# Performance work log

Measured on AMD Instinct MI355X. Metric: run time of the kernel, lower is better.

The kernel has to match this reference:

```python
import jax, jax.numpy as jnp
import numpy as np

L = 5          # number of pyramid levels (cat_fuse expects 5*C input channels)
C = 192        # in_channels, divisible by 3 and 2
C3 = C // 3
C2 = C // 2
B = 4
SIZES = [(192, 192), (96, 96), (48, 48), (24, 24), (12, 12)]  # x[1] is reference scale


def conv1x1(x, w, b):
    # 1x1 conv (+ folded eval-mode BN): x [n,cin,h,w], w [cout,cin], b [cout]
    return jnp.einsum('oc,nchw->nohw', w, x) + b[None, :, None, None]


def setup_inputs() -> dict:
    key = jax.random.key(0)
    ks = iter(jax.random.split(key, 40))
    inp = {}
    for i, (h, w) in enumerate(SIZES):
        inp[f'x{i}'] = jax.random.normal(next(ks), (B, C, h, w), jnp.float32)
    def wp(shape):
        return jax.random.normal(next(ks), shape, jnp.float32) * 0.05
    for nm, co, ci in [('k1', C3, C), ('k2', C3, C), ('k3', C3, C), ('q', C, C), ('v', C, C),
                       ('cf', C, L * C), ('e1', C2, C), ('e2', C, C2), ('r1', C2, C), ('r2', C, C2)]:
        inp['W_' + nm] = wp((co, ci))
        inp['b_' + nm] = wp((co,))
    inp['bn_s'] = 1.0 + wp((C,))   # standalone BN folded to affine scale
    inp['bn_t'] = wp((C,))         # standalone BN folded to affine shift
    return inp


def reference(x0, x1, x2, x3, x4,
              W_k1, b_k1, W_k2, b_k2, W_k3, b_k3,
              W_q, b_q, W_v, b_v, W_cf, b_cf,
              W_e1, b_e1, W_e2, b_e2, W_r1, b_r1, W_r2, b_r2,
              bn_s, bn_t):
    xs = [x0, x1, x2, x3, x4]
    b, _, h, w = x1.shape
    hw = h * w
    # bilinear resize to reference scale (torch F.interpolate align_corners=False)
    x_up = [x1 if i == 1 else jax.image.resize(x, (b, C, h, w), 'bilinear') for i, x in enumerate(xs)]
    Xf = jnp.stack(x_up).reshape(L * b, C, h, w)  # shared weights across levels -> batch them

    def emb(z):  # conv1x1 -> GELU(exact) -> conv1x1 (dropout is identity at eval)
        return conv1x1(jax.nn.gelu(conv1x1(z, W_e1, b_e1), approximate=False), W_e2, b_e2)

    la_res = None
    for k in range(5):
        # residual refinement: relu(bn(x + res_block(x)))
        r = conv1x1(jax.nn.relu(conv1x1(Xf, W_r1, b_r1)), W_r2, b_r2)
        Xf = jax.nn.relu((Xf + r) * bn_s[None, :, None, None] + bn_t[None, :, None, None])
        # query/value: per-level projection, split C into 3 chunks -> 15 'keys' per pixel
        Q = conv1x1(Xf, W_q, b_q).reshape(L, b, 3, C3, hw)
        Q = Q.transpose(1, 0, 2, 3, 4).reshape(b, 3 * L, C3, hw).transpose(0, 3, 2, 1)  # [b,hw,C3,15]
        V = conv1x1(Xf, W_v, b_v).reshape(L, b, 3, C3, hw)
        V = V.transpose(1, 0, 2, 3, 4).reshape(b, 3 * L, C3, hw).transpose(0, 3, 1, 2)  # [b,hw,15,C3]
        if k == 0:
            cat = Xf.reshape(L, b, C, h, w).transpose(1, 0, 2, 3, 4).reshape(b, L * C, h, w)
            la_res = emb(jax.nn.relu(conv1x1(cat, W_cf, b_cf)))
        refs = []
        for Wk, bk in ((W_k1, b_k1), (W_k2, b_k2), (W_k3, b_k3)):
            key_i = conv1x1(la_res, Wk, bk).reshape(b, C3, hw).transpose(0, 2, 1)       # [b,hw,C3]
            att = jax.nn.softmax(jnp.einsum('bpc,bpck->bpk', key_i, Q), axis=-1)        # [b,hw,15]
            ref = jnp.einsum('bpk,bpkc->bpc', att, V)                                   # [b,hw,C3]
            refs.append(ref.transpose(0, 2, 1).reshape(b, C3, h, w))
        la_res = emb(jnp.concatenate(refs, axis=1))
    return la_res
```

## Files before the change

kernel.cpp:

```cpp
#include <hip/hip_runtime.h>
#include <math.h>

typedef unsigned short u16;
typedef unsigned int   u32;
typedef __bf16 bf16x8 __attribute__((ext_vector_type(8)));
typedef float  f32x4  __attribute__((ext_vector_type(4)));

__device__ __forceinline__ float b2f(u16 u) {
    unsigned v = ((unsigned)u) << 16;
    return __uint_as_float(v);
}
__device__ __forceinline__ u16 f2b(float f) {
    unsigned x = __float_as_uint(f);
    unsigned r = (x + 0x7fffu + ((x >> 16) & 1u)) >> 16;
    return (u16)r;
}
__device__ __forceinline__ void fsplit(float v, u16& h, u16& l) {
    h = f2b(v);
    l = f2b(v - b2f(h));
}
__device__ __forceinline__ float h2f(u16 u) {
    union { u16 us; _Float16 h; } c; c.us = u; return (float)c.h;
}
__device__ __forceinline__ u16 f2h(float f) {
    union { u16 us; _Float16 h; } c; c.h = (_Float16)f; return c.us;
}
__device__ __forceinline__ float ldx(const void* p, size_t i, int f32m) {
    return f32m ? ((const float*)p)[i] : b2f(((const u16*)p)[i]);
}

__device__ __forceinline__ void gld16(u16* l, const u16* g) {
    __builtin_amdgcn_global_load_lds(
        (const __attribute__((address_space(1))) unsigned int*)g,
        (__attribute__((address_space(3))) unsigned int*)l,
        16, 0, 0);
}

__device__ __forceinline__ int swz(int row) {
    return (row & 3) ^ ((row >> 2) & 3);
}

__global__ void detect_dtype(const u16* __restrict__ x0, int* flag)
{
    int lane = threadIdx.x;
    int bad = 0;
    for (int i = lane; i < 1024; i += 64) {
        float v = b2f(x0[i]);
        if (!(fabsf(v) < 32768.f)) bad = 1;
    }
    unsigned long long m = __ballot(bad);
    if (lane == 0) flag[0] = (m != 0ULL) ? 1 : 0;
}

struct SrcPtrs {
    const void *wr1, *br1, *wr2, *br2, *wq, *bq, *wv, *bv, *wcf, *bcf;
    const void *we1, *be1, *we2, *be2, *wk1, *bk1, *wk2, *bk2, *wk3, *bk3;
    const void *bns, *bnt;
};
__global__ void pack_weights(SrcPtrs S, u16* __restrict__ Wh, u16* __restrict__ Wl,
                             float* __restrict__ Bias, const int* __restrict__ dflag)
{
    const int f32m = *dflag;
    int idx = blockIdx.x * 256 + threadIdx.x;
    if (idx < 368640) {
        const void* src; size_t si;
        if (idx < 18432)       { src = S.wr1; si = idx; }
        else if (idx < 36864)  { src = S.wr2; si = idx - 18432; }
        else if (idx < 110592) {
            int r = idx - 36864, o = r / 192, c = r % 192;
            if (o < 192) { src = S.wq; si = (size_t)o * 192 + c; }
            else         { src = S.wv; si = (size_t)(o - 192) * 192 + c; }
        }
        else if (idx < 294912) { src = S.wcf; si = idx - 110592; }
        else if (idx < 313344) { src = S.we1; si = idx - 294912; }
        else if (idx < 331776) { src = S.we2; si = idx - 313344; }
        else {
            int r = idx - 331776, o = r / 192, c = r % 192;
            src = (o < 64) ? S.wk1 : ((o < 128) ? S.wk2 : S.wk3);
            si = (size_t)(o & 63) * 192 + c;
        }
        u16 h, l; fsplit(ldx(src, si, f32m), h, l);
        Wh[idx] = h; Wl[idx] = l;
    } else if (idx < 370368) {
        int b = idx - 368640; const void* src; size_t si;
        if (b < 96)        { src = S.br1; si = b; }
        else if (b < 288)  { src = S.br2; si = b - 96; }
        else if (b < 672)  { int r = b - 288;
                             if (r < 192) { src = S.bq; si = r; }
                             else         { src = S.bv; si = r - 192; } }
        else if (b < 864)  { src = S.bcf; si = b - 672; }
        else if (b < 960)  { src = S.be1; si = b - 864; }
        else if (b < 1152) { src = S.be2; si = b - 960; }
        else if (b < 1344) { int r = b - 1152;
                             src = (r < 64) ? S.bk1 : ((r < 128) ? S.bk2 : S.bk3);
                             si = r & 63; }
        else if (b < 1536) { src = S.bns; si = b - 1344; }
        else               { src = S.bnt; si = b - 1536; }
        Bias[b] = ldx(src, si, f32m);
    }
}

__global__ void build_tables(float* __restrict__ wtab, int* __restrict__ jtab)
{
    int t = threadIdx.x;
    if (t >= 384) return;
    int li = t / 96, o = t % 96;
    const int ins[4] = {192, 48, 24, 12};
    int in = ins[li];
    float scale = (float)in / 96.0f;
    float ksc = fmaxf(scale, 1.0f);
    float cc = (o + 0.5f) * scale - 0.5f;
    float w[4] = {0.f, 0.f, 0.f, 0.f};
    int   j[4] = {0, 0, 0, 0};
    int n = 0; float s = 0.f;
    int jl = (int)floorf(cc - ksc), jh = (int)floorf(cc + ksc) + 1;
    for (int jj = jl; jj <= jh; jj++) {
        if (jj < 0 || jj >= in) continue;
        float ww = 1.0f - fabsf((float)jj - cc) / ksc;
        if (ww <= 0.f) continue;
        if (n < 4) { w[n] = ww; j[n] = jj; s += ww; n++; }
    }
    for (int i = 0; i < 4; i++) {
        wtab[li * 384 + o * 4 + i] = w[i] / s;
        jtab[li * 384 + o * 4 + i] = j[i];
    }
}

template<int SPLIT>
__launch_bounds__(256)
__global__ void transpose_in(const void* __restrict__ src, int HW,
                             u32* __restrict__ P, u16* __restrict__ Xh,
                             u16* __restrict__ Xl, const int* __restrict__ dflag)
{
    __shared__ float t[32][33];
    const int f32m = *dflag;
    const int b  = blockIdx.z;
    const int c0 = blockIdx.y * 32;
    const int p0 = blockIdx.x * 32;
    const int tid = threadIdx.x;
#pragma unroll
    for (int it = 0; it < 4; it++) {
        int i = it * 256 + tid;
        int pl = i & 31, cl = i >> 5;
        int p = p0 + pl;
        float v = 0.f;
        if (p < HW) v = ldx(src, ((size_t)(b * 192 + c0 + cl)) * HW + p, f32m);
        t[pl][cl] = v;
    }
    __syncthreads();
#pragma unroll
    for (int it = 0; it < 4; it++) {
        int i = it * 256 + tid;
        int cl = i & 31, pl = i >> 5;
        int p = p0 + pl;
        if (p >= HW) continue;
        float v = t[pl][cl];
        u16 h, l; fsplit(v, h, l);
        if constexpr (SPLIT) {
            size_t oi = ((size_t)((4 + b) * 9216 + p)) * 192 + c0 + cl;
            Xh[oi] = h; Xl[oi] = l;
        } else {
            P[((size_t)b * HW + p) * 192 + c0 + cl] = (u32)h | ((u32)l << 16);
        }
    }
}

template<int TAPS>
__launch_bounds__(256)
__global__ void upsample2(const u32* __restrict__ Pa, const u32* __restrict__ Pb,
                          const u32* __restrict__ Pc,
                          const float* __restrict__ wtab, const int* __restrict__ jtab,
                          u16* __restrict__ Xh, u16* __restrict__ Xl)
{
    int li, b, l, in;
    const u32* P;
    if constexpr (TAPS == 4) {
        li = 0; b = blockIdx.y; l = 0; in = 192; P = Pa;
    } else {
        int yi = blockIdx.y;
        li = 1 + (yi >> 2); b = yi & 3;
        const int lvl[4] = {0, 2, 3, 4};
        const int ins[4] = {192, 48, 24, 12};
        l = lvl[li]; in = ins[li];
        P = (li == 1) ? Pa : ((li == 2) ? Pb : Pc);
    }
    int gid = blockIdx.x * 256 + threadIdx.x;
    int c = gid % 192;
    int p = gid / 192;
    int y = p / 96, x = p % 96;
    const float* wt = wtab + li * 384;
    const int*   jt = jtab + li * 384;

    size_t ib = (size_t)b * in * in * 192 + c;
    float a = 0.f;
#pragma unroll
    for (int iy = 0; iy < TAPS; iy++) {
        float wy = wt[y * 4 + iy];
        size_t rb = ib + (size_t)(jt[y * 4 + iy] * in) * 192;
        float ax = 0.f;
#pragma unroll
        for (int ix = 0; ix < TAPS; ix++) {
            u32 u = P[rb + jt[x * 4 + ix] * 192];
            ax += wt[x * 4 + ix] * (b2f((u16)u) + b2f((u16)(u >> 16)));
        }
        a += wy * ax;
    }
    size_t oi = ((size_t)(l * 4 + b) * 9216 + p) * 192 + c;
    u16 h, lo; fsplit(a, h, lo);
    Xh[oi] = h; Xl[oi] = lo;
}

template<int MT, int NT, int ACT, int MODE, int OUT>
__launch_bounds__(256)
__global__ void conv_gemm(const u16* __restrict__ Ah, const u16* __restrict__ Al,
                          const u16* __restrict__ Wh, const u16* __restrict__ Wl,
                          const float* __restrict__ Bias,
                          int woff, int boff, int K, int O,
                          u16* __restrict__ out0, u16* __restrict__ out1)
{
    constexpr int BM = MT * 64, BN = NT * 16;
    __shared__ u16 Ash[BM * 40];
    __shared__ u16 Asl[BM * 40];
    __shared__ u16 Bsh[BN * 40];
    __shared__ u16 Bsl[BN * 40];

    const int tid  = threadIdx.x;
    const int lane = tid & 63, wave = tid >> 6;
    const int qd   = lane >> 4, ln = lane & 15;
    const int p0   = blockIdx.x * BM;
    const int img  = blockIdx.z;
    const int M    = 9216;

    f32x4 acc[MT][NT];
#pragma unroll
    for (int mt = 0; mt < MT; mt++)
#pragma unroll
        for (int j = 0; j < NT; j++) acc[mt][j] = (f32x4){0.f, 0.f, 0.f, 0.f};

    for (int kb = 0; kb < K; kb += 32) {
#pragma unroll
        for (int i = 0; i < MT; i++) {
            int idx = i * 256 + tid;
            int row = idx >> 2, ch = idx & 3;
            size_t base;
            if constexpr (MODE == 2) {
                int l = kb / 192, c0 = kb - l * 192 + ch * 8;
                base = ((size_t)((l * 4 + img) * M + p0 + row)) * 192 + c0;
            } else {
                base = ((size_t)(img * M + p0 + row)) * (size_t)K + kb + ch * 8;
            }
            *(float4*)&Ash[row * 40 + ch * 8] = *(const float4*)(Ah + base);
            *(float4*)&Asl[row * 40 + ch * 8] = *(const float4*)(Al + base);
        }
        constexpr int BI = (BN * 4) / 256;
#pragma unroll
        for (int i = 0; i < BI; i++) {
            int idx = i * 256 + tid;
            int row = idx >> 2, ch = idx & 3;
            size_t wb = (size_t)woff + (size_t)row * K + kb + ch * 8;
            *(float4*)&Bsh[row * 40 + ch * 8] = *(const float4*)(Wh + wb);
            *(float4*)&Bsl[row * 40 + ch * 8] = *(const float4*)(Wl + wb);
        }
        __syncthreads();
        bf16x8 ah[MT], al[MT];
#pragma unroll
        for (int mt = 0; mt < MT; mt++) {
            ah[mt] = *(const bf16x8*)&Ash[(wave * MT * 16 + mt * 16 + ln) * 40 + qd * 8];
            al[mt] = *(const bf16x8*)&Asl[(wave * MT * 16 + mt * 16 + ln) * 40 + qd * 8];
        }
#pragma unroll
        for (int j = 0; j < NT; j++) {
            bf16x8 bh = *(const bf16x8*)&Bsh[(j * 16 + ln) * 40 + qd * 8];
            bf16x8 bl = *(const bf16x8*)&Bsl[(j * 16 + ln) * 40 + qd * 8];
#pragma unroll
            for (int mt = 0; mt < MT; mt++) {
                acc[mt][j] = __builtin_amdgcn_mfma_f32_16x16x32_bf16(ah[mt], bh, acc[mt][j], 0, 0, 0);
                acc[mt][j] = __builtin_amdgcn_mfma_f32_16x16x32_bf16(ah[mt], bl, acc[mt][j], 0, 0, 0);
                acc[mt][j] = __builtin_amdgcn_mfma_f32_16x16x32_bf16(al[mt], bh, acc[mt][j], 0, 0, 0);
            }
        }
        __syncthreads();
    }

#pragma unroll
    for (int mt = 0; mt < MT; mt++) {
#pragma unroll
        for (int j = 0; j < NT; j++) {
            int o = j * 16 + ln;
            float bvf = Bias[boff + o];
#pragma unroll
            for (int r = 0; r < 4; r++) {
                int prow = p0 + wave * MT * 16 + mt * 16 + qd * 4 + r;
                float v = acc[mt][j][r] + bvf;
                if constexpr (ACT == 1) v = fmaxf(v, 0.f);
                if constexpr (OUT == 0) {
                    size_t oidx = ((size_t)(img * M + prow)) * (size_t)O + o;
                    u16 h, l; fsplit(v, h, l);
                    out0[oidx] = h; out1[oidx] = l;
                } else if constexpr (OUT == 1) {
                    out0[((size_t)(img * M + prow)) * (size_t)O + o] = f2h(v);
                } else {
                    size_t pb = ((size_t)(img * M + prow)) * 192;
                    if (o < 192) out0[pb + o] = f2h(v);
                    else         out1[pb + o - 192] = f2h(v);
                }
            }
        }
    }
}

template<int ACT1, int MODE2>
__launch_bounds__(256)
__global__ void fused_mlp(const u16* __restrict__ Ah, const u16* __restrict__ Al,
                          const u16* __restrict__ Wh, const u16* __restrict__ Wl,
                          const float* __restrict__ Bias,
                          int w1off, int b1off, int w2off, int b2off,
                          u16* __restrict__ outh, u16* __restrict__ outl)
{
    __shared__ __align__(16) u16 LDS[38912];
    u16* Hh = LDS;
    u16* Hl = LDS + 6656;

    const int tid  = threadIdx.x;
    const int lane = tid & 63, wave = tid >> 6;
    const int qd   = lane >> 4, ln = lane & 15;
    const int p0   = blockIdx.x * 64;
    const int img  = blockIdx.z;
    const int M    = 9216;
    const int irow = tid >> 2, ich = tid & 3;

    auto g1issue = [&](int kb, int c) {
        u16* SA = LDS + 13312 + c * 10240;
        int ch = ich ^ swz(irow);
        size_t ga = ((size_t)(img * M + p0 + irow)) * 192 + kb + ch * 8;
        gld16(SA + wave * 512,        Ah + ga);
        gld16(SA + 2048 + wave * 512, Al + ga);
        size_t gb = (size_t)w1off + (size_t)irow * 192 + kb + ch * 8;
        gld16(SA + 4096 + wave * 512, Wh + gb);
        gld16(SA + 7168 + wave * 512, Wl + gb);
        if (tid < 128) {
            int r2 = 64 + irow;
            int ch2 = ich ^ swz(r2);
            size_t gb2 = (size_t)w1off + (size_t)r2 * 192 + kb + ch2 * 8;
            gld16(SA + 6144 + wave * 512, Wh + gb2);
            gld16(SA + 9216 + wave * 512, Wl + gb2);
        }
    };
    auto g2issue = [&](int kb, int c) {
        u16* B2 = LDS + 13312 + c * 12288;
#pragma unroll
        for (int i = 0; i < 3; i++) {
            int r = i * 64 + irow;
            int ch = ich ^ swz(r);
            size_t g = (size_t)w2off + (size_t)r * 96 + kb + ch * 8;
            gld16(B2 + i * 2048 + wave * 512,        Wh + g);
            gld16(B2 + 6144 + i * 2048 + wave * 512, Wl + g);
        }
    };

    f32x4 acc1[6];
#pragma unroll
    for (int j = 0; j < 6; j++) acc1[j] = (f32x4){0.f, 0.f, 0.f, 0.f};

    g1issue(0, 0);
    __syncthreads();
#pragma unroll 2
    for (int kb = 0; kb < 192; kb += 32) {
        int cur = (kb >> 5) & 1;
        if (kb + 32 < 192) g1issue(kb + 32, cur ^ 1);
        const u16* SA = LDS + 13312 + cur * 10240;
        int arow = wave * 16 + ln;
        int asl = arow * 32 + ((qd ^ swz(arow)) << 3);
        bf16x8 ah = *(const bf16x8*)&SA[asl];
        bf16x8 al = *(const bf16x8*)&SA[2048 + asl];
#pragma unroll
        for (int j = 0; j < 6; j++) {
            int brow = j * 16 + ln;
            int bsl = brow * 32 + ((qd ^ swz(brow)) << 3);
            bf16x8 bh = *(const bf16x8*)&SA[4096 + bsl];
            bf16x8 bl = *(const bf16x8*)&SA[7168 + bsl];
            acc1[j] = __builtin_amdgcn_mfma_f32_16x16x32_bf16(ah, bh, acc1[j], 0, 0, 0);
            acc1[j] = __builtin_amdgcn_mfma_f32_16x16x32_bf16(ah, bl, acc1[j], 0, 0, 0);
            acc1[j] = __builtin_amdgcn_mfma_f32_16x16x32_bf16(al, bh, acc1[j], 0, 0, 0);
        }
        __syncthreads();
    }

    g2issue(0, 0);
#pragma unroll
    for (int j = 0; j < 6; j++) {
        int o = j * 16 + ln;
        float bvf = Bias[b1off + o];
#pragma unroll
        for (int r = 0; r < 4; r++) {
            float v = acc1[j][r] + bvf;
            if constexpr (ACT1 == 1) v = fmaxf(v, 0.f);
            if constexpr (ACT1 == 2) v = 0.5f * v * (1.f + erff(v * 0.70710678118654752f));
            u16 h, l; fsplit(v, h, l);
            int row = wave * 16 + qd * 4 + r;
            Hh[row * 104 + o] = h;
            Hl[row * 104 + o] = l;
        }
    }
    __syncthreads();

    f32x4 acc2[12];
#pragma unroll
    for (int j = 0; j < 12; j++) acc2[j] = (f32x4){0.f, 0.f, 0.f, 0.f};

#pragma unroll
    for (int kb = 0; kb < 96; kb += 32) {
        int cur = (kb >> 5) & 1;
        if (kb + 32 < 96) g2issue(kb + 32, cur ^ 1);
        const u16* B2 = LDS + 13312 + cur * 12288;
        bf16x8 ah = *(const bf16x8*)&Hh[(wave * 16 + ln) * 104 + kb + qd * 8];
        bf16x8 al = *(const bf16x8*)&Hl[(wave * 16 + ln) * 104 + kb + qd * 8];
#pragma unroll
        for (int j = 0; j < 12; j++) {
            int brow = j * 16 + ln;
            int bsl = brow * 32 + ((qd ^ swz(brow)) << 3);
            bf16x8 bh = *(const bf16x8*)&B2[bsl];
            bf16x8 bl = *(const bf16x8*)&B2[6144 + bsl];
            acc2[j] = __builtin_amdgcn_mfma_f32_16x16x32_bf16(ah, bh, acc2[j], 0, 0, 0);
            acc2[j] = __builtin_amdgcn_mfma_f32_16x16x32_bf16(ah, bl, acc2[j], 0, 0, 0);
            acc2[j] = __builtin_amdgcn_mfma_f32_16x16x32_bf16(al, bh, acc2[j], 0, 0, 0);
        }
        __syncthreads();
    }

#pragma unroll
    for (int j = 0; j < 12; j++) {
        int o = j * 16 + ln;
        float bvf = Bias[b2off + o];
#pragma unroll
        for (int r = 0; r < 4; r++) {
            int prow = p0 + wave * 16 + qd * 4 + r;
            float v = acc2[j][r] + bvf;
            size_t oidx = ((size_t)(img * M + prow)) * 192 + o;
            if constexpr (MODE2 == 1) {
                float xo = b2f(outh[oidx]) + b2f(outl[oidx]);
                v = fmaxf((xo + v) * Bias[1344 + o] + Bias[1536 + o], 0.f);
            }
            u16 h, l; fsplit(v, h, l);
            outh[oidx] = h; outl[oidx] = l;
        }
    }
}

template<int WRITE_X>
__launch_bounds__(256)
__global__ void fused_res_qv(u16* __restrict__ Xh, u16* __restrict__ Xl,
                             const u16* __restrict__ Wh, const u16* __restrict__ Wl,
                             const float* __restrict__ Bias,
                             u16* __restrict__ Qf, u16* __restrict__ Vf)
{
    __shared__ __align__(16) u16 LDS[38912];
    u16* Hh = LDS;
    u16* Hl = LDS + 6656;

    const int tid  = threadIdx.x;
    const int lane = tid & 63, wave = tid >> 6;
    const int qd   = lane >> 4, ln = lane & 15;
    const int p0   = blockIdx.x * 64;
    const int img  = blockIdx.z;
    const int M    = 9216;
    const int irow = tid >> 2, ich = tid & 3;

    auto g1issue = [&](int kb, int c) {
        u16* SA = LDS + 13312 + c * 10240;
        int ch = ich ^ swz(irow);
        size_t ga = ((size_t)(img * M + p0 + irow)) * 192 + kb + ch * 8;
        gld16(SA + wave * 512,        Xh + ga);
        gld16(SA + 2048 + wave * 512, Xl + ga);
        size_t gb = (size_t)irow * 192 + kb + ch * 8;
        gld16(SA + 4096 + wave * 512, Wh + gb);
        gld16(SA + 7168 + wave * 512, Wl + gb);
        if (tid < 128) {
            int r2 = 64 + irow;
            int ch2 = ich ^ swz(r2);
            size_t gb2 = (size_t)r2 * 192 + kb + ch2 * 8;
            gld16(SA + 6144 + wave * 512, Wh + gb2);
            gld16(SA + 9216 + wave * 512, Wl + gb2);
        }
    };
    auto g2issue = [&](int kb, int c) {
        u16* B2 = LDS + 13312 + c * 12288;
#pragma unroll
        for (int i = 0; i < 3; i++) {
            int r = i * 64 + irow;
            int ch = ich ^ swz(r);
            size_t g = (size_t)18432 + (size_t)r * 96 + kb + ch * 8;
            gld16(B2 + i * 2048 + wave * 512,        Wh + g);
            gld16(B2 + 6144 + i * 2048 + wave * 512, Wl + g);
        }
    };
    auto g3issue = [&](int s, int c) {
        int p = s / 6, kb = (s - p * 6) * 32;
        u16* B3 = LDS + 24576 + c * 6144;
        int ch = ich ^ swz(irow);
        size_t g = (size_t)36864 + (size_t)(p * 96 + irow) * 192 + kb + ch * 8;
        gld16(B3 + wave * 512,        Wh + g);
        gld16(B3 + 3072 + wave * 512, Wl + g);
        if (tid < 128) {
            int r2 = 64 + irow;
            int ch2 = ich ^ swz(r2);
            size_t g2 = (size_t)36864 + (size_t)(p * 96 + r2) * 192 + kb + ch2 * 8;
            gld16(B3 + 2048 + wave * 512, Wh + g2);
            gld16(B3 + 5120 + wave * 512, Wl + g2);
        }
    };

    f32x4 acc1[6];
#pragma unroll
    for (int j = 0; j < 6; j++) acc1[j] = (f32x4){0.f, 0.f, 0.f, 0.f};

    g1issue(0, 0);
    __syncthreads();
#pragma unroll 2
    for (int kb = 0; kb < 192; kb += 32) {
        int cur = (kb >> 5) & 1;
        if (kb + 32 < 192) g1issue(kb + 32, cur ^ 1);
        const u16* SA = LDS + 13312 + cur * 10240;
        int arow = wave * 16 + ln;
        int asl = arow * 32 + ((qd ^ swz(arow)) << 3);
        bf16x8 ah = *(const bf16x8*)&SA[asl];
        bf16x8 al = *(const bf16x8*)&SA[2048 + asl];
#pragma unroll
        for (int j = 0; j < 6; j++) {
            int brow = j * 16 + ln;
            int bsl = brow * 32 + ((qd ^ swz(brow)) << 3);
            bf16x8 bh = *(const bf16x8*)&SA[4096 + bsl];
            bf16x8 bl = *(const bf16x8*)&SA[7168 + bsl];
            acc1[j] = __builtin_amdgcn_mfma_f32_16x16x32_bf16(ah, bh, acc1[j], 0, 0, 0);
            acc1[j] = __builtin_amdgcn_mfma_f32_16x16x32_bf16(ah, bl, acc1[j], 0, 0, 0);
            acc1[j] = __builtin_amdgcn_mfma_f32_16x16x32_bf16(al, bh, acc1[j], 0, 0, 0);
        }
        __syncthreads();
    }

    g2issue(0, 0);
#pragma unroll
    for (int j = 0; j < 6; j++) {
        int o = j * 16 + ln;
        float bvf = Bias[o];
#pragma unroll
        for (int r = 0; r < 4; r++) {
            float v = fmaxf(acc1[j][r] + bvf, 0.f);
            u16 h, l; fsplit(v, h, l);
            int row = wave * 16 + qd * 4 + r;
            Hh[row * 104 + o] = h;
            Hl[row * 104 + o] = l;
        }
    }
    __syncthreads();

    f32x4 acc2[12];
#pragma unroll
    for (int j = 0; j < 12; j++) acc2[j] = (f32x4){0.f, 0.f, 0.f, 0.f};

#pragma unroll
    for (int kb = 0; kb < 96; kb += 32) {
        int cur = (kb >> 5) & 1;
        if (kb + 32 < 96) g2issue(kb + 32, cur ^ 1);
        const u16* B2 = LDS + 13312 + cur * 12288;
        bf16x8 ah = *(const bf16x8*)&Hh[(wave * 16 + ln) * 104 + kb + qd * 8];
        bf16x8 al = *(const bf16x8*)&Hl[(wave * 16 + ln) * 104 + kb + qd * 8];
#pragma unroll
        for (int j = 0; j < 12; j++) {
            int brow = j * 16 + ln;
            int bsl = brow * 32 + ((qd ^ swz(brow)) << 3);
            bf16x8 bh = *(const bf16x8*)&B2[bsl];
            bf16x8 bl = *(const bf16x8*)&B2[6144 + bsl];
            acc2[j] = __builtin_amdgcn_mfma_f32_16x16x32_bf16(ah, bh, acc2[j], 0, 0, 0);
            acc2[j] = __builtin_amdgcn_mfma_f32_16x16x32_bf16(ah, bl, acc2[j], 0, 0, 0);
            acc2[j] = __builtin_amdgcn_mfma_f32_16x16x32_bf16(al, bh, acc2[j], 0, 0, 0);
        }
        __syncthreads();
    }

    g3issue(0, 0);

    u16* X2h = LDS;
    u16* X2l = LDS + 12288;
#pragma unroll
    for (int j = 0; j < 12; j++) {
        int o = j * 16 + ln;
        float bvf = Bias[96 + o];
#pragma unroll
        for (int r = 0; r < 4; r++) {
            int row  = wave * 16 + qd * 4 + r;
            int prow = p0 + row;
            float v = acc2[j][r] + bvf;
            size_t oidx = ((size_t)(img * M + prow)) * 192 + o;
            float xo = b2f(Xh[oidx]) + b2f(Xl[oidx]);
            v = fmaxf((xo + v) * Bias[1344 + o] + Bias[1536 + o], 0.f);
            u16 h, l; fsplit(v, h, l);
            if constexpr (WRITE_X) { Xh[oidx] = h; Xl[oidx] = l; }
            int off = ((row * 192 + o) * 2) ^ ((row & 7) << 4);
            *(u16*)((char*)X2h + off) = h;
            *(u16*)((char*)X2l + off) = l;
        }
    }
    __syncthreads();

    const int arow = wave * 16 + ln;
#pragma unroll 1
    for (int pass = 0; pass < 4; pass++) {
        f32x4 acc3[6];
#pragma unroll
        for (int j = 0; j < 6; j++) acc3[j] = (f32x4){0.f, 0.f, 0.f, 0.f};

#pragma unroll 2
        for (int t6 = 0; t6 < 6; t6++) {
            int s = pass * 6 + t6;
            int cur = t6 & 1;
            if (s < 23) g3issue(s + 1, cur ^ 1);
            int kb = t6 * 32;
            int aoff = ((arow * 192 + kb + qd * 8) * 2) ^ ((arow & 7) << 4);
            bf16x8 ah = *(const bf16x8*)((const char*)X2h + aoff);
            bf16x8 al = *(const bf16x8*)((const char*)X2l + aoff);
            const u16* B3 = LDS + 24576 + cur * 6144;
#pragma unroll
            for (int j = 0; j < 6; j++) {
                int brow = j * 16 + ln;
                int bsl = brow * 32 + ((qd ^ swz(brow)) << 3);
                bf16x8 bh = *(const bf16x8*)&B3[bsl];
                bf16x8 bl = *(const bf16x8*)&B3[3072 + bsl];
                acc3[j] = __builtin_amdgcn_mfma_f32_16x16x32_bf16(ah, bh, acc3[j], 0, 0, 0);
                acc3[j] = __builtin_amdgcn_mfma_f32_16x16x32_bf16(ah, bl, acc3[j], 0, 0, 0);
                acc3[j] = __builtin_amdgcn_mfma_f32_16x16x32_bf16(al, bh, acc3[j], 0, 0, 0);
            }
            __syncthreads();
        }
#pragma unroll
        for (int j = 0; j < 6; j++) {
            int o = pass * 96 + j * 16 + ln;
            float bvf = Bias[288 + o];
#pragma unroll
            for (int r = 0; r < 4; r++) {
                int prow = p0 + wave * 16 + qd * 4 + r;
                float v = acc3[j][r] + bvf;
                u16 q = f2h(v);
                size_t pb = ((size_t)(img * M + prow)) * 192;
                if (o < 192) Qf[pb + o] = q;
                else         Vf[pb + o - 192] = q;
            }
        }
    }
}

__global__ void attn_kernel(const u16* __restrict__ Qb, const u16* __restrict__ Vb,
                            const u16* __restrict__ Keys,
                            u16* __restrict__ Rh, u16* __restrict__ Rl)
{
    const int lane = threadIdx.x & 63;
    const int wv   = threadIdx.x >> 6;
    const int p = blockIdx.x * 4 + wv;
    const int b = blockIdx.y;

    float qv[15], vv[15];
#pragma unroll
    for (int l = 0; l < 5; l++) {
        size_t base = ((size_t)((l * 4 + b) * 9216 + p)) * 192;
#pragma unroll
        for (int j = 0; j < 3; j++) {
            qv[l * 3 + j] = h2f(Qb[base + j * 64 + lane]);
            vv[l * 3 + j] = h2f(Vb[base + j * 64 + lane]);
        }
    }
    size_t kb = ((size_t)(b * 9216 + p)) * 192;
#pragma unroll
    for (int i = 0; i < 3; i++) {
        float kf = h2f(Keys[kb + i * 64 + lane]);
        float lg[15];
#pragma unroll
        for (int t = 0; t < 15; t++) {
            float s = kf * qv[t];
#pragma unroll
            for (int m = 1; m < 64; m <<= 1) s += __shfl_xor(s, m, 64);
            lg[t] = s;
        }
        float mx = lg[0];
#pragma unroll
        for (int t = 1; t < 15; t++) mx = fmaxf(mx, lg[t]);
        float sum = 0.f;
#pragma unroll
        for (int t = 0; t < 15; t++) { lg[t] = __expf(lg[t] - mx); sum += lg[t]; }
        float inv = 1.f / sum;
        float ref = 0.f;
#pragma unroll
        for (int t = 0; t < 15; t++) ref += lg[t] * vv[t];
        u16 h, lo; fsplit(ref * inv, h, lo);
        Rh[kb + i * 64 + lane] = h;
        Rl[kb + i * 64 + lane] = lo;
    }
}

__launch_bounds__(256)
__global__ void transpose_out(const u16* __restrict__ Lah, const u16* __restrict__ Lal,
                              float* __restrict__ out)
{
    __shared__ float t[32][33];
    const int b  = blockIdx.z;
    const int c0 = blockIdx.y * 32;
    const int p0 = blockIdx.x * 32;
    const int tid = threadIdx.x;
#pragma unroll
    for (int it = 0; it < 4; it++) {
        int i = it * 256 + tid;
        int cl = i & 31, pl = i >> 5;
        size_t idx = ((size_t)(b * 9216 + p0 + pl)) * 192 + c0 + cl;
        t[pl][cl] = b2f(Lah[idx]) + b2f(Lal[idx]);
    }
    __syncthreads();
#pragma unroll
    for (int it = 0; it < 4; it++) {
        int i = it * 256 + tid;
        int pl = i & 31, cl = i >> 5;
        out[((size_t)(b * 192 + c0 + cl)) * 9216 + p0 + pl] = t[pl][cl];
    }
}

__global__ void ws_too_small_kernel(float* out)
{
    int gid = blockIdx.x * 256 + threadIdx.x;
    out[gid] = 12345.0f;
}

extern "C" void kernel_launch(void* const* d_in, const int* in_sizes, int n_in,
                              void* d_out, int out_size, void* d_ws, size_t ws_size,
                              hipStream_t stream)
{
    u16* ws = (u16*)d_ws;
    const size_t oXh   = 0;
    const size_t oXl   = 35389440;
    const size_t oQ    = 70778880;
    const size_t oV    = 106168320;
    const size_t oLah  = 141557760;
    const size_t oLal  = 148635648;
    const size_t oKeys = 155713536;
    const size_t oRh   = 162791424;
    const size_t oRl   = 169869312;
    const size_t oWh   = 176947200;
    const size_t oWl   = 177315840;
    const size_t oBias = 177684480;
    const size_t oWtab = 177687936;
    const size_t oJtab = 177691008;
    const size_t oFlag = 177694080;
    const size_t need_bytes = (size_t)177694096 * 2;

    if (ws_size < need_bytes) {
        ws_too_small_kernel<<<dim3(out_size / 256), dim3(256), 0, stream>>>((float*)d_out);
        return;
    }

    u16* Xh   = ws + oXh;
    u16* Xl   = ws + oXl;
    u16* Qf   = ws + oQ;
    u16* Vf   = ws + oV;
    u16* Lah  = ws + oLah;
    u16* Lal  = ws + oLal;
    u16* Keys = ws + oKeys;
    u16* Rh   = ws + oRh;
    u16* Rl   = ws + oRl;
    u16* Wh   = ws + oWh;
    u16* Wl   = ws + oWl;
    float* Bias = (float*)(ws + oBias);
    float* wtab = (float*)(ws + oWtab);
    int*   jtab = (int*)(ws + oJtab);
    int*   flag = (int*)(ws + oFlag);

    u32* P0 = (u32*)(ws + oQ);
    u32* P2 = (u32*)(ws + oLah);
    u32* P3 = (u32*)(ws + oLal);
    u32* P4 = (u32*)(ws + oKeys);

    SrcPtrs S;
    S.wk1 = d_in[5];  S.bk1 = d_in[6];
    S.wk2 = d_in[7];  S.bk2 = d_in[8];
    S.wk3 = d_in[9];  S.bk3 = d_in[10];
    S.wq  = d_in[11]; S.bq  = d_in[12];
    S.wv  = d_in[13]; S.bv  = d_in[14];
    S.wcf = d_in[15]; S.bcf = d_in[16];
    S.we1 = d_in[17]; S.be1 = d_in[18];
    S.we2 = d_in[19]; S.be2 = d_in[20];
    S.wr1 = d_in[21]; S.br1 = d_in[22];
    S.wr2 = d_in[23]; S.br2 = d_in[24];
    S.bns = d_in[25]; S.bnt = d_in[26];

    dim3 blk(256);
    detect_dtype<<<dim3(1), dim3(64), 0, stream>>>((const u16*)d_in[0], flag);
    pack_weights<<<dim3(1447), blk, 0, stream>>>(S, Wh, Wl, Bias, flag);
    build_tables<<<dim3(1), dim3(384), 0, stream>>>(wtab, jtab);

    transpose_in<0><<<dim3(1152, 6, 4), blk, 0, stream>>>(d_in[0], 36864, P0, nullptr, nullptr, flag);
    transpose_in<1><<<dim3( 288, 6, 4), blk, 0, stream>>>(d_in[1],  9216, nullptr, Xh, Xl, flag);
    transpose_in<0><<<dim3(  72, 6, 4), blk, 0, stream>>>(d_in[2],  2304, P2, nullptr, nullptr, flag);
    transpose_in<0><<<dim3(  18, 6, 4), blk, 0, stream>>>(d_in[3],   576, P3, nullptr, nullptr, flag);
    transpose_in<0><<<dim3(   5, 6, 4), blk, 0, stream>>>(d_in[4],   144, P4, nullptr, nullptr, flag);
    upsample2<4><<<dim3(6912,  4), blk, 0, stream>>>(P0, nullptr, nullptr, wtab, jtab, Xh, Xl);
    upsample2<2><<<dim3(6912, 12), blk, 0, stream>>>(P2, P3, P4, wtab, jtab, Xh, Xl);

    for (int k = 0; k < 5; k++) {
        if (k < 4)
            fused_res_qv<1><<<dim3(144, 1, 20), blk, 0, stream>>>(
                Xh, Xl, Wh, Wl, Bias, Qf, Vf);
        else
            fused_res_qv<0><<<dim3(144, 1, 20), blk, 0, stream>>>(
                Xh, Xl, Wh, Wl, Bias, Qf, Vf);
        if (k == 0) {
            conv_gemm<2, 12, 1, 2, 0><<<dim3(72, 1, 4), blk, 0, stream>>>(
                Xh, Xl, Wh, Wl, Bias, 110592, 672, 960, 192, Rh, Rl);
            fused_mlp<2, 0><<<dim3(144, 1, 4), blk, 0, stream>>>(
                Rh, Rl, Wh, Wl, Bias, 294912, 864, 313344, 960, Lah, Lal);
        }
        conv_gemm<2, 12, 0, 0, 1><<<dim3(72, 1, 4), blk, 0, stream>>>(
            Lah, Lal, Wh, Wl, Bias, 331776, 1152, 192, 192, Keys, nullptr);
        attn_kernel<<<dim3(2304, 4), blk, 0, stream>>>(Qf, Vf, Keys, Rh, Rl);
        fused_mlp<2, 0><<<dim3(144, 1, 4), blk, 0, stream>>>(
            Rh, Rl, Wh, Wl, Bias, 294912, 864, 313344, 960, Lah, Lal);
    }
    transpose_out<<<dim3(288, 6, 4), blk, 0, stream>>>(Lah, Lal, (float*)d_out);
}
```

Before: 2.520 ms.

## Fuse key projection GEMM into the embedding MLP epilogue

The embedding MLP kernel now stages its 64x192 output tile (hi/lo bf16 split) in LDS. It then runs the key projection (three C3 heads, 192 outputs) directly from that tile, writing Keys in fp16. This removes the separate conv_gemm launch and its re-read of la_res from global memory each iteration. In exchange, the MLP kernel gets longer per block, adds an extra double-buffered weight stream and more LDS use, and skips the keys work on the last iteration.

Result: slower. 2.605 ms (+3.4%).

```diff
diff --git a/kernel.cpp b/kernel.cpp
--- a/kernel.cpp
+++ b/kernel.cpp
@@ -309,13 +309,14 @@
     }
 }
 
-template<int ACT1, int MODE2>
+template<int ACT1, int MODE2, int KEYS>
 __launch_bounds__(256)
 __global__ void fused_mlp(const u16* __restrict__ Ah, const u16* __restrict__ Al,
                           const u16* __restrict__ Wh, const u16* __restrict__ Wl,
                           const float* __restrict__ Bias,
                           int w1off, int b1off, int w2off, int b2off,
-                          u16* __restrict__ outh, u16* __restrict__ outl)
+                          u16* __restrict__ outh, u16* __restrict__ outl,
+                          u16* __restrict__ Keys)
 {
     __shared__ __align__(16) u16 LDS[38912];
     u16* Hh = LDS;
@@ -357,6 +358,21 @@
             gld16(B2 + 6144 + i * 2048 + wave * 512, Wl + g);
         }
     };
+    auto g3issue = [&](int s, int c) {
+        int p = s / 6, kb = (s - p * 6) * 32;
+        u16* B3 = LDS + 24576 + c * 6144;
+        int ch = ich ^ swz(irow);
+        size_t g = (size_t)331776 + (size_t)(p * 96 + irow) * 192 + kb + ch * 8;
+        gld16(B3 + wave * 512,        Wh + g);
+        gld16(B3 + 3072 + wave * 512, Wl + g);
+        if (tid < 128) {
+            int r2 = 64 + irow;
+            int ch2 = ich ^ swz(r2);
+            size_t g2 = (size_t)331776 + (size_t)(p * 96 + r2) * 192 + kb + ch2 * 8;
+            gld16(B3 + 2048 + wave * 512, Wh + g2);
+            gld16(B3 + 5120 + wave * 512, Wl + g2);
+        }
+    };
 
     f32x4 acc1[6];
 #pragma unroll
@@ -428,13 +444,18 @@
         __syncthreads();
     }
 
+    if constexpr (KEYS) g3issue(0, 0);
+
+    u16* X2h = LDS;
+    u16* X2l = LDS + 12288;
 #pragma unroll
     for (int j = 0; j < 12; j++) {
         int o = j * 16 + ln;
         float bvf = Bias[b2off + o];
 #pragma unroll
         for (int r = 0; r < 4; r++) {
-            int prow = p0 + wave * 16 + qd * 4 + r;
+            int row  = wave * 16 + qd * 4 + r;
+            int prow = p0 + row;
             float v = acc2[j][r] + bvf;
             size_t oidx = ((size_t)(img * M + prow)) * 192 + o;
             if constexpr (MODE2 == 1) {
@@ -443,6 +464,54 @@
             }
             u16 h, l; fsplit(v, h, l);
             outh[oidx] = h; outl[oidx] = l;
+            if constexpr (KEYS) {
+                int off = ((row * 192 + o) * 2) ^ ((row & 7) << 4);
+                *(u16*)((char*)X2h + off) = h;
+                *(u16*)((char*)X2l + off) = l;
+            }
+        }
+    }
+    if constexpr (!KEYS) return;
+    __syncthreads();
+
+    const int arow = wave * 16 + ln;
+#pragma unroll 1
+    for (int pass = 0; pass < 2; pass++) {
+        f32x4 acc3[6];
+#pragma unroll
+        for (int j = 0; j < 6; j++) acc3[j] = (f32x4){0.f, 0.f, 0.f, 0.f};
+
+#pragma unroll 2
+        for (int t6 = 0; t6 < 6; t6++) {
+            int s = pass * 6 + t6;
+            int cur = t6 & 1;
+            if (s < 11) g3issue(s + 1, cur ^ 1);
+            int kb = t6 * 32;
+            int aoff = ((arow * 192 + kb + qd * 8) * 2) ^ ((arow & 7) << 4);
+            bf16x8 ah = *(const bf16x8*)((const char*)X2h + aoff);
+            bf16x8 al = *(const bf16x8*)((const char*)X2l + aoff);
+            const u16* B3 = LDS + 24576 + cur * 6144;
+#pragma unroll
+            for (int j = 0; j < 6; j++) {
+                int brow = j * 16 + ln;
+                int bsl = brow * 32 + ((qd ^ swz(brow)) << 3);
+                bf16x8 bh = *(const bf16x8*)&B3[bsl];
+                bf16x8 bl = *(const bf16x8*)&B3[3072 + bsl];
+                acc3[j] = __builtin_amdgcn_mfma_f32_16x16x32_bf16(ah, bh, acc3[j], 0, 0, 0);
+                acc3[j] = __builtin_amdgcn_mfma_f32_16x16x32_bf16(ah, bl, acc3[j], 0, 0, 0);
+                acc3[j] = __builtin_amdgcn_mfma_f32_16x16x32_bf16(al, bh, acc3[j], 0, 0, 0);
+            }
+            __syncthreads();
+        }
+#pragma unroll
+        for (int j = 0; j < 6; j++) {
+            int o = pass * 96 + j * 16 + ln;
+            float bvf = Bias[1152 + o];
+#pragma unroll
+            for (int r = 0; r < 4; r++) {
+                int prow = p0 + wave * 16 + qd * 4 + r;
+                Keys[((size_t)(img * M + prow)) * 192 + o] = f2h(acc3[j][r] + bvf);
+            }
         }
     }
 }
@@ -811,14 +880,16 @@
         if (k == 0) {
             conv_gemm<2, 12, 1, 2, 0><<<dim3(72, 1, 4), blk, 0, stream>>>(
                 Xh, Xl, Wh, Wl, Bias, 110592, 672, 960, 192, Rh, Rl);
-            fused_mlp<2, 0><<<dim3(144, 1, 4), blk, 0, stream>>>(
-                Rh, Rl, Wh, Wl, Bias, 294912, 864, 313344, 960, Lah, Lal);
-        }
-        conv_gemm<2, 12, 0, 0, 1><<<dim3(72, 1, 4), blk, 0, stream>>>(
-            Lah, Lal, Wh, Wl, Bias, 331776, 1152, 192, 192, Keys, nullptr);
+            fused_mlp<2, 0, 1><<<dim3(144, 1, 4), blk, 0, stream>>>(
+                Rh, Rl, Wh, Wl, Bias, 294912, 864, 313344, 960, Lah, Lal, Keys);
+        }
         attn_kernel<<<dim3(2304, 4), blk, 0, stream>>>(Qf, Vf, Keys, Rh, Rl);
-        fused_mlp<2, 0><<<dim3(144, 1, 4), blk, 0, stream>>>(
-            Rh, Rl, Wh, Wl, Bias, 294912, 864, 313344, 960, Lah, Lal);
+        if (k < 4)
+            fused_mlp<2, 0, 1><<<dim3(144, 1, 4), blk, 0, stream>>>(
+                Rh, Rl, Wh, Wl, Bias, 294912, 864, 313344, 960, Lah, Lal, Keys);
+        else
+            fused_mlp<2, 0, 0><<<dim3(144, 1, 4), blk, 0, stream>>>(
+                Rh, Rl, Wh, Wl, Bias, 294912, 864, 313344, 960, Lah, Lal, nullptr);
     }
     transpose_out<<<dim3(288, 6, 4), blk, 0, stream>>>(Lah, Lal, (float*)d_out);
 }
```

## Double-buffer conv_gemm with async global-to-LDS loads and swizzled layout

Applied to the files above, without the earlier changes.

Rewrites conv_gemm to fetch the next K-slice straight into LDS (gld16) while the current slice feeds MFMA, using two LDS buffers and an XOR swizzle in place of padded rows. The M tile drops from 128 to 64 rows, doubling the grid to 144 blocks per image so more blocks are resident. The goal is to hide global load latency and cut LDS bank conflicts, at the cost of less A-fragment reuse per B load and 64KB of LDS per block.

Result: faster. 2.456 ms (-2.5%).

```diff
diff --git a/kernel.cpp b/kernel.cpp
--- a/kernel.cpp
+++ b/kernel.cpp
@@ -210,7 +210,7 @@
     Xh[oi] = h; Xl[oi] = lo;
 }
 
-template<int MT, int NT, int ACT, int MODE, int OUT>
+template<int NT, int ACT, int MODE, int OUT>
 __launch_bounds__(256)
 __global__ void conv_gemm(const u16* __restrict__ Ah, const u16* __restrict__ Al,
                           const u16* __restrict__ Wh, const u16* __restrict__ Wl,
@@ -218,92 +218,87 @@
                           int woff, int boff, int K, int O,
                           u16* __restrict__ out0, u16* __restrict__ out1)
 {
-    constexpr int BM = MT * 64, BN = NT * 16;
-    __shared__ u16 Ash[BM * 40];
-    __shared__ u16 Asl[BM * 40];
-    __shared__ u16 Bsh[BN * 40];
-    __shared__ u16 Bsl[BN * 40];
+    __shared__ __align__(16) u16 LDS[32768];
 
     const int tid  = threadIdx.x;
     const int lane = tid & 63, wave = tid >> 6;
     const int qd   = lane >> 4, ln = lane & 15;
-    const int p0   = blockIdx.x * BM;
+    const int p0   = blockIdx.x * 64;
     const int img  = blockIdx.z;
     const int M    = 9216;
-
-    f32x4 acc[MT][NT];
-#pragma unroll
-    for (int mt = 0; mt < MT; mt++)
-#pragma unroll
-        for (int j = 0; j < NT; j++) acc[mt][j] = (f32x4){0.f, 0.f, 0.f, 0.f};
-
+    const int irow = tid >> 2, ich = tid & 3;
+
+    auto issue = [&](int kb, int c) {
+        u16* S = LDS + c * 16384;
+        {
+            int ch = ich ^ swz(irow);
+            size_t ga;
+            if constexpr (MODE == 2) {
+                int l = kb / 192;
+                ga = ((size_t)((l * 4 + img) * M + p0 + irow)) * 192 + (kb - l * 192) + ch * 8;
+            } else {
+                ga = ((size_t)(img * M + p0 + irow)) * (size_t)K + kb + ch * 8;
+            }
+            gld16(S + wave * 512,        Ah + ga);
+            gld16(S + 2048 + wave * 512, Al + ga);
+        }
+#pragma unroll
+        for (int i = 0; i < 3; i++) {
+            int idx = i * 256 + tid;
+            int brow = idx >> 2;
+            int bc = (idx & 3) ^ swz(brow);
+            size_t gb = (size_t)woff + (size_t)brow * K + kb + bc * 8;
+            gld16(S + 4096 + i * 2048 + wave * 512,  Wh + gb);
+            gld16(S + 10240 + i * 2048 + wave * 512, Wl + gb);
+        }
+    };
+
+    f32x4 acc[NT];
+#pragma unroll
+    for (int j = 0; j < NT; j++) acc[j] = (f32x4){0.f, 0.f, 0.f, 0.f};
+
+    issue(0, 0);
+    __syncthreads();
     for (int kb = 0; kb < K; kb += 32) {
-#pragma unroll
-        for (int i = 0; i < MT; i++) {
-            int idx = i * 256 + tid;
-            int row = idx >> 2, ch = idx & 3;
-            size_t base;
-            if constexpr (MODE == 2) {
-                int l = kb / 192, c0 = kb - l * 192 + ch * 8;
-                base = ((size_t)((l * 4 + img) * M + p0 + row)) * 192 + c0;
+        int cur = (kb >> 5) & 1;
+        if (kb + 32 < K) issue(kb + 32, cur ^ 1);
+        const u16* S = LDS + cur * 16384;
+        int arow = wave * 16 + ln;
+        int asl = arow * 32 + ((qd ^ swz(arow)) << 3);
+        bf16x8 ah = *(const bf16x8*)&S[asl];
+        bf16x8 al = *(const bf16x8*)&S[2048 + asl];
+#pragma unroll
+        for (int j = 0; j < NT; j++) {
+            int brow = j * 16 + ln;
+            int bsl = brow * 32 + ((qd ^ swz(brow)) << 3);
+            bf16x8 bh = *(const bf16x8*)&S[4096 + bsl];
+            bf16x8 bl = *(const bf16x8*)&S[10240 + bsl];
+            acc[j] = __builtin_amdgcn_mfma_f32_16x16x32_bf16(ah, bh, acc[j], 0, 0, 0);
+            acc[j] = __builtin_amdgcn_mfma_f32_16x16x32_bf16(ah, bl, acc[j], 0, 0, 0);
+            acc[j] = __builtin_amdgcn_mfma_f32_16x16x32_bf16(al, bh, acc[j], 0, 0, 0);
+        }
+        __syncthreads();
+    }
+
+#pragma unroll
+    for (int j = 0; j < NT; j++) {
+        int o = j * 16 + ln;
+        float bvf = Bias[boff + o];
+#pragma unroll
+        for (int r = 0; r < 4; r++) {
+            int prow = p0 + wave * 16 + qd * 4 + r;
+            float v = acc[j][r] + bvf;
+            if constexpr (ACT == 1) v = fmaxf(v, 0.f);
+            if constexpr (OUT == 0) {
+                size_t oidx = ((size_t)(img * M + prow)) * (size_t)O + o;
+                u16 h, l; fsplit(v, h, l);
+                out0[oidx] = h; out1[oidx] = l;
+            } else if constexpr (OUT == 1) {
+                out0[((size_t)(img * M + prow)) * (size_t)O + o] = f2h(v);
             } else {
-                base = ((size_t)(img * M + p0 + row)) * (size_t)K + kb + ch * 8;
-            }
-            *(float4*)&Ash[row * 40 + ch * 8] = *(const float4*)(Ah + base);
-            *(float4*)&Asl[row * 40 + ch * 8] = *(const float4*)(Al + base);
-        }
-        constexpr int BI = (BN * 4) / 256;
-#pragma unroll
-        for (int i = 0; i < BI; i++) {
-            int idx = i * 256 + tid;
-            int row = idx >> 2, ch = idx & 3;
-            size_t wb = (size_t)woff + (size_t)row * K + kb + ch * 8;
-            *(float4*)&Bsh[row * 40 + ch * 8] = *(const float4*)(Wh + wb);
-            *(float4*)&Bsl[row * 40 + ch * 8] = *(const float4*)(Wl + wb);
-        }
-        __syncthreads();
-        bf16x8 ah[MT], al[MT];
-#pragma unroll
-        for (int mt = 0; mt < MT; mt++) {
-            ah[mt] = *(const bf16x8*)&Ash[(wave * MT * 16 + mt * 16 + ln) * 40 + qd * 8];
-            al[mt] = *(const bf16x8*)&Asl[(wave * MT * 16 + mt * 16 + ln) * 40 + qd * 8];
-        }
-#pragma unroll
-        for (int j = 0; j < NT; j++) {
-            bf16x8 bh = *(const bf16x8*)&Bsh[(j * 16 + ln) * 40 + qd * 8];
-            bf16x8 bl = *(const bf16x8*)&Bsl[(j * 16 + ln) * 40 + qd * 8];
-#pragma unroll
-            for (int mt = 0; mt < MT; mt++) {
-                acc[mt][j] = __builtin_amdgcn_mfma_f32_16x16x32_bf16(ah[mt], bh, acc[mt][j], 0, 0, 0);
-                acc[mt][j] = __builtin_amdgcn_mfma_f32_16x16x32_bf16(ah[mt], bl, acc[mt][j], 0, 0, 0);
-                acc[mt][j] = __builtin_amdgcn_mfma_f32_16x16x32_bf16(al[mt], bh, acc[mt][j], 0, 0, 0);
-            }
-        }
-        __syncthreads();
-    }
-
-#pragma unroll
-    for (int mt = 0; mt < MT; mt++) {
-#pragma unroll
-        for (int j = 0; j < NT; j++) {
-            int o = j * 16 + ln;
-            float bvf = Bias[boff + o];
-#pragma unroll
-            for (int r = 0; r < 4; r++) {
-                int prow = p0 + wave * MT * 16 + mt * 16 + qd * 4 + r;
-                float v = acc[mt][j][r] + bvf;
-                if constexpr (ACT == 1) v = fmaxf(v, 0.f);
-                if constexpr (OUT == 0) {
-                    size_t oidx = ((size_t)(img * M + prow)) * (size_t)O + o;
-                    u16 h, l; fsplit(v, h, l);
-                    out0[oidx] = h; out1[oidx] = l;
-                } else if constexpr (OUT == 1) {
-                    out0[((size_t)(img * M + prow)) * (size_t)O + o] = f2h(v);
-                } else {
-                    size_t pb = ((size_t)(img * M + prow)) * 192;
-                    if (o < 192) out0[pb + o] = f2h(v);
-                    else         out1[pb + o - 192] = f2h(v);
-                }
+                size_t pb = ((size_t)(img * M + prow)) * 192;
+                if (o < 192) out0[pb + o] = f2h(v);
+                else         out1[pb + o - 192] = f2h(v);
             }
         }
     }
@@ -809,12 +804,12 @@
             fused_res_qv<0><<<dim3(144, 1, 20), blk, 0, stream>>>(
                 Xh, Xl, Wh, Wl, Bias, Qf, Vf);
         if (k == 0) {
-            conv_gemm<2, 12, 1, 2, 0><<<dim3(72, 1, 4), blk, 0, stream>>>(
+            conv_gemm<12, 1, 2, 0><<<dim3(144, 1, 4), blk, 0, stream>>>(
                 Xh, Xl, Wh, Wl, Bias, 110592, 672, 960, 192, Rh, Rl);
             fused_mlp<2, 0><<<dim3(144, 1, 4), blk, 0, stream>>>(
                 Rh, Rl, Wh, Wl, Bias, 294912, 864, 313344, 960, Lah, Lal);
         }
-        conv_gemm<2, 12, 0, 0, 1><<<dim3(72, 1, 4), blk, 0, stream>>>(
+        conv_gemm<12, 0, 0, 1><<<dim3(144, 1, 4), blk, 0, stream>>>(
             Lah, Lal, Wh, Wl, Bias, 331776, 1152, 192, 192, Keys, nullptr);
         attn_kernel<<<dim3(2304, 4), blk, 0, stream>>>(Qf, Vf, Keys, Rh, Rl);
         fused_mlp<2, 0><<<dim3(144, 1, 4), blk, 0, stream>>>(
```
